# Optimization experiments

Hardware: AMD Instinct MI355X
Metric: run time of the kernel (lower is better)

Reference implementation:

```python
import jax, jax.numpy as jnp
import numpy as np

N_NODES = 20000
N_EDGES = 320000
F_IN = 256      # num_features_mol
HIDDEN = 512    # hidden_size


def _glorot(key, shape):
    fan_in, fan_out = shape
    lim = jnp.sqrt(6.0 / (fan_in + fan_out)).astype(jnp.float32)
    return jax.random.uniform(key, shape, jnp.float32, -lim, lim)


def setup_inputs() -> dict:
    key = jax.random.key(0)
    ks = jax.random.split(key, 12)
    x = jax.random.normal(ks[0], (N_NODES, F_IN), jnp.float32)
    edge_index = jax.random.randint(ks[1], (2, N_EDGES), 0, N_NODES, dtype=jnp.int64)
    d1, d2, d3 = F_IN * 2, F_IN * 2, F_IN * 4  # 512, 512, 1024
    return {
        "x": x,
        "edge_index": edge_index,
        # SAGEConv layer i: lin_l (neighbor, with bias), lin_r (root, no bias)
        "Wl1": _glorot(ks[2], (F_IN, d1)), "bl1": jnp.zeros((d1,), jnp.float32),
        "Wr1": _glorot(ks[3], (F_IN, d1)),
        "Wl2": _glorot(ks[4], (d1, d2)), "bl2": jnp.zeros((d2,), jnp.float32),
        "Wr2": _glorot(ks[5], (d1, d2)),
        "Wl3": _glorot(ks[6], (d2, d3)), "bl3": jnp.zeros((d3,), jnp.float32),
        "Wr3": _glorot(ks[7], (d2, d3)),
        # mol_fc_g1: Linear(4*F -> hidden)
        "Wfc": _glorot(ks[8], (d3, HIDDEN)), "bfc": jnp.zeros((HIDDEN,), jnp.float32),
    }


def _sage_mean(x, src, dst, Wl, bl, Wr):
    # mean-aggregate neighbor features: messages flow src -> dst
    msg = x[src]                                               # [E, d]
    agg = jax.ops.segment_sum(msg, dst, num_segments=N_NODES)  # [N, d]
    cnt = jax.ops.segment_sum(jnp.ones((src.shape[0],), x.dtype), dst,
                              num_segments=N_NODES)            # [N]
    mean = agg / jnp.maximum(cnt, 1.0)[:, None]                # zero-deg -> 0
    return mean @ Wl + bl + x @ Wr


def reference(x, edge_index, Wl1, bl1, Wr1, Wl2, bl2, Wr2, Wl3, bl3, Wr3, Wfc, bfc):
    src, dst = edge_index[0], edge_index[1]
    h = jax.nn.relu(_sage_mean(x, src, dst, Wl1, bl1, Wr1))
    h = jax.nn.relu(_sage_mean(h, src, dst, Wl2, bl2, Wr2))
    h = jax.nn.relu(_sage_mean(h, src, dst, Wl3, bl3, Wr3))
    return h @ Wfc + bfc                                       # [N, HIDDEN]
```

## Files before the change

### kernel.cpp

```cpp
#include <hip/hip_runtime.h>
#include <hip/hip_bf16.h>


typedef __bf16 bf16x8 __attribute__((ext_vector_type(8)));
typedef float  f32x4  __attribute__((ext_vector_type(4)));

#define N_NODES 20000
#define N_EDGES 320000

__device__ __forceinline__ int clampi(int v, int lo, int hi) {
    return v < lo ? lo : (v > hi ? hi : v);
}

__device__ __forceinline__ void load16_lds(const void* g, void* l) {
    __builtin_amdgcn_global_load_lds(
        (const __attribute__((address_space(1))) void*)g,
        (__attribute__((address_space(3))) void*)l, 16, 0, 0);
}


__global__ void k_count(const int* __restrict__ ei, int E, int* __restrict__ cnt) {
    int e = blockIdx.x * blockDim.x + threadIdx.x;
    if (e < E) {
        int dst = clampi(ei[E + e], 0, N_NODES - 1);
        atomicAdd(&cnt[dst], 1);
    }
}

__global__ __launch_bounds__(1024) void k_scan_block(const int* __restrict__ cnt,
                                                     int* __restrict__ off,
                                                     int* __restrict__ bsum, int n) {
    __shared__ int sm[1024];
    int b = blockIdx.x, tid = threadIdx.x;
    int i = b * 1024 + tid;
    int v = (i < n) ? cnt[i] : 0;
    sm[tid] = v;
    __syncthreads();
    for (int s = 1; s < 1024; s <<= 1) {
        int t = (tid >= s) ? sm[tid - s] : 0;
        __syncthreads();
        sm[tid] += t;
        __syncthreads();
    }
    if (i < n) off[i] = sm[tid] - v;
    if (tid == 1023) bsum[b] = sm[1023];
}

__global__ void k_scan_carry(const int* __restrict__ bsum, int* __restrict__ carry,
                             int nb, int* __restrict__ off, int n) {
    if (threadIdx.x == 0 && blockIdx.x == 0) {
        int acc = 0;
        for (int b = 0; b < nb; ++b) { carry[b] = acc; acc += bsum[b]; }
        off[n] = acc;
    }
}

__global__ __launch_bounds__(1024) void k_scan_add(int* __restrict__ off,
                                                   int* __restrict__ cur,
                                                   const int* __restrict__ carry, int n) {
    int i = blockIdx.x * 1024 + threadIdx.x;
    if (i < n) {
        int v = off[i] + carry[blockIdx.x];
        off[i] = v;
        cur[i] = v;
    }
}

__global__ void k_fill(const int* __restrict__ ei, int E,
                       int* __restrict__ cur, int* __restrict__ csr) {
    int e = blockIdx.x * blockDim.x + threadIdx.x;
    if (e < E) {
        int dst = clampi(ei[E + e], 0, N_NODES - 1);
        int src = clampi(ei[e], 0, N_NODES - 1);
        int pos = atomicAdd(&cur[dst], 1);
        if (pos >= 0 && pos < E) csr[pos] = src;
    }
}


__global__ void k_transpose_w(const float* __restrict__ W, int K, int N,
                              __hip_bfloat16* __restrict__ Wt, int ldt, int koff) {
    __shared__ float tile[32][33];
    int kb = blockIdx.y * 32, nb = blockIdx.x * 32;
    for (int i = 0; i < 32; i += 8) {
        int k = kb + threadIdx.y + i, n = nb + threadIdx.x;
        tile[threadIdx.y + i][threadIdx.x] = W[(size_t)k * N + n];
    }
    __syncthreads();
    for (int i = 0; i < 32; i += 8) {
        int n = nb + threadIdx.y + i, k = kb + threadIdx.x;
        Wt[(size_t)n * ldt + koff + k] = __float2bfloat16(tile[threadIdx.x][threadIdx.y + i]);
    }
}


__global__ __launch_bounds__(256) void k_agg_f32(const float* __restrict__ xin,
                                                 const int* __restrict__ off,
                                                 const int* __restrict__ csr,
                                                 __hip_bfloat16* __restrict__ outp,
                                                 int ostride) {
    __shared__ float sm[4][256];
    int node = blockIdx.x;
    int tid = threadIdx.x;
    int slot = tid >> 6, lane = tid & 63;
    int c0 = lane * 4;
    int beg = off[node], end = off[node + 1];
    float a0 = 0.f, a1 = 0.f, a2 = 0.f, a3 = 0.f;
    for (int e = beg + slot; e < end; e += 4) {
        int s = csr[e];
        float4 v = *(const float4*)(xin + (size_t)s * 256 + c0);
        a0 += v.x; a1 += v.y; a2 += v.z; a3 += v.w;
    }
    sm[slot][c0] = a0; sm[slot][c0 + 1] = a1; sm[slot][c0 + 2] = a2; sm[slot][c0 + 3] = a3;
    __syncthreads();
    float inv = 1.f / fmaxf((float)(end - beg), 1.f);
    float r = (sm[0][tid] + sm[1][tid]) + (sm[2][tid] + sm[3][tid]);
    outp[(size_t)node * ostride + tid] = __float2bfloat16(r * inv);
    outp[(size_t)node * ostride + 256 + tid] = __float2bfloat16(xin[(size_t)node * 256 + tid]);
}

__global__ __launch_bounds__(256) void k_agg_bf16(const __hip_bfloat16* __restrict__ hin,
                                                  int istride,
                                                  const int* __restrict__ off,
                                                  const int* __restrict__ csr,
                                                  __hip_bfloat16* __restrict__ outp,
                                                  int ostride) {
    __shared__ float sm[4][512];
    int node = blockIdx.x;
    int tid = threadIdx.x;
    int slot = tid >> 6, lane = tid & 63;
    int c0 = lane * 8;
    int beg = off[node], end = off[node + 1];
    float a[8] = {};
    for (int e = beg + slot; e < end; e += 4) {
        int s = csr[e];
        uint4 v = *(const uint4*)(hin + (size_t)s * istride + c0);
        const __hip_bfloat16* hb = (const __hip_bfloat16*)&v;
#pragma unroll
        for (int j = 0; j < 8; ++j) a[j] += __bfloat162float(hb[j]);
    }
#pragma unroll
    for (int j = 0; j < 8; ++j) sm[slot][c0 + j] = a[j];
    __syncthreads();
    float inv = 1.f / fmaxf((float)(end - beg), 1.f);
    int c = tid * 2;
    float r0 = (sm[0][c] + sm[1][c]) + (sm[2][c] + sm[3][c]);
    float r1 = (sm[0][c + 1] + sm[1][c + 1]) + (sm[2][c + 1] + sm[3][c + 1]);
    __hip_bfloat162 o;
    o.x = __float2bfloat16(r0 * inv);
    o.y = __float2bfloat16(r1 * inv);
    *(__hip_bfloat162*)(outp + (size_t)node * ostride + c) = o;
}


#define SMEM_BYTES 34816

template <bool RELU, bool OUT_BF16>
__global__ __launch_bounds__(256) void k_gemm_bt(const __hip_bfloat16* __restrict__ A,
                                                 int lda, int M, int K,
                                                 const __hip_bfloat16* __restrict__ Bt,
                                                 const float* __restrict__ bias,
                                                 __hip_bfloat16* __restrict__ obf,
                                                 float* __restrict__ of32,
                                                 int ldc, int coff,
                                                 int rtiles, int ctlog2) {
    __shared__ char smem[SMEM_BYTES];
    __bf16* Alds = (__bf16*)smem;
    __bf16* Blds = (__bf16*)(smem + 8192);

    int bid = blockIdx.x;
    int xcd = bid & 7, local = bid >> 3;
    int cmask = (1 << ctlog2) - 1;
    int colTile = local & cmask;
    int rowTile = (local >> ctlog2) * 8 + xcd;
    if (rowTile >= rtiles) return;
    int row0 = rowTile * 128, col0 = colTile * 128;

    int tid = threadIdx.x;
    int wave = tid >> 6, lane = tid & 63;
    int wr = wave >> 1, wc = wave & 1;
    int quad = lane >> 4, l16 = lane & 15;

    int rlo = lane >> 2, ch = lane & 3;
    int ra0 = clampi(row0 + wave * 32 + rlo, 0, M - 1);
    int ra1 = clampi(row0 + wave * 32 + 16 + rlo, 0, M - 1);
    const __hip_bfloat16* gA0 = A + (size_t)ra0 * lda + ch * 8;
    const __hip_bfloat16* gA1 = A + (size_t)ra1 * lda + ch * 8;
    const __hip_bfloat16* gB0 = Bt + (size_t)(col0 + wave * 32 + rlo) * K + ch * 8;
    const __hip_bfloat16* gB1 = gB0 + (size_t)16 * K;
    __bf16* lA0 = Alds + (wave * 32) * 32;
    __bf16* lA1 = Alds + (wave * 32 + 16) * 32;
    __bf16* lB0 = Blds + (wave * 32) * 32;
    __bf16* lB1 = Blds + (wave * 32 + 16) * 32;

    f32x4 acc[4][4] = {};

    for (int k0 = 0; k0 < K; k0 += 32) {
        __syncthreads();
        load16_lds(gA0 + k0, lA0);
        load16_lds(gA1 + k0, lA1);
        load16_lds(gB0 + k0, lB0);
        load16_lds(gB1 + k0, lB1);
        __syncthreads();

        bf16x8 af[4], bf[4];
#pragma unroll
        for (int mi = 0; mi < 4; ++mi)
            af[mi] = *(const bf16x8*)(Alds + (wr * 64 + mi * 16 + l16) * 32 + quad * 8);
#pragma unroll
        for (int ni = 0; ni < 4; ++ni)
            bf[ni] = *(const bf16x8*)(Blds + (wc * 64 + ni * 16 + l16) * 32 + quad * 8);
#pragma unroll
        for (int mi = 0; mi < 4; ++mi)
#pragma unroll
            for (int ni = 0; ni < 4; ++ni)
                acc[mi][ni] = __builtin_amdgcn_mfma_f32_16x16x32_bf16(af[mi], bf[ni],
                                                                      acc[mi][ni], 0, 0, 0);
    }

    __syncthreads();
    if (OUT_BF16) {
        __bf16* cb = (__bf16*)smem;
#pragma unroll
        for (int ni = 0; ni < 4; ++ni) {
            int ct = wc * 64 + ni * 16 + l16;
            float bv = bias[col0 + ct];
#pragma unroll
            for (int mi = 0; mi < 4; ++mi) {
                int rb = wr * 64 + mi * 16 + quad * 4;
#pragma unroll
                for (int r = 0; r < 4; ++r) {
                    float v = acc[mi][ni][r] + bv;
                    if (RELU) v = fmaxf(v, 0.f);
                    cb[(rb + r) * 136 + ct] = (__bf16)v;
                }
            }
        }
        __syncthreads();
        int chunk = tid & 15;
        int rl = tid >> 4;
#pragma unroll
        for (int p = 0; p < 8; ++p) {
            int rt = p * 16 + rl;
            int row = row0 + rt;
            if (row < M) {
                uint4 v = *(const uint4*)(cb + rt * 136 + chunk * 8);
                *(uint4*)(obf + (size_t)row * ldc + coff + col0 + chunk * 8) = v;
            }
        }
    } else {
        float* cf = (float*)smem;
#pragma unroll
        for (int h = 0; h < 2; ++h) {
            if (wc == h) {
#pragma unroll
                for (int ni = 0; ni < 4; ++ni) {
                    int ctl = ni * 16 + l16;
                    float bv = bias[col0 + h * 64 + ctl];
#pragma unroll
                    for (int mi = 0; mi < 4; ++mi) {
                        int rb = wr * 64 + mi * 16 + quad * 4;
#pragma unroll
                        for (int r = 0; r < 4; ++r) {
                            float v = acc[mi][ni][r] + bv;
                            if (RELU) v = fmaxf(v, 0.f);
                            cf[(rb + r) * 68 + ctl] = v;
                        }
                    }
                }
            }
            __syncthreads();
            int chunk = tid & 15;
            int rl = tid >> 4;
#pragma unroll
            for (int p = 0; p < 8; ++p) {
                int rt = p * 16 + rl;
                int row = row0 + rt;
                if (row < M) {
                    float4 v = *(const float4*)(cf + rt * 68 + chunk * 4);
                    *(float4*)(of32 + (size_t)row * ldc + col0 + h * 64 + chunk * 4) = v;
                }
            }
            __syncthreads();
        }
    }
}


extern "C" void kernel_launch(void* const* d_in, const int* in_sizes, int n_in,
                              void* d_out, int out_size, void* d_ws, size_t ws_size,
                              hipStream_t stream) {
    const float* x   = (const float*)d_in[0];
    const int*   ei  = (const int*)d_in[1];
    const float* Wl1 = (const float*)d_in[2];
    const float* bl1 = (const float*)d_in[3];
    const float* Wr1 = (const float*)d_in[4];
    const float* Wl2 = (const float*)d_in[5];
    const float* bl2 = (const float*)d_in[6];
    const float* Wr2 = (const float*)d_in[7];
    const float* Wl3 = (const float*)d_in[8];
    const float* bl3 = (const float*)d_in[9];
    const float* Wr3 = (const float*)d_in[10];
    const float* Wfc = (const float*)d_in[11];
    const float* bfc = (const float*)d_in[12];
    float* out = (float*)d_out;

    const int NN = N_NODES, E = N_EDGES;
    const int NB = (NN + 1023) / 1024;

    char* p = (char*)d_ws;
    auto alloc = [&](size_t bytes) {
        char* r = p;
        p += (bytes + 511) & ~(size_t)511;
        return r;
    };
    int* cnt   = (int*)alloc((size_t)NN * 4);
    int* off   = (int*)alloc((size_t)(NN + 1) * 4);
    int* cur   = (int*)alloc((size_t)NN * 4);
    int* csr   = (int*)alloc((size_t)E * 4);
    int* bsum  = (int*)alloc((size_t)NB * 4);
    int* carry = (int*)alloc((size_t)NB * 4);
    __hip_bfloat16* Acat1 = (__hip_bfloat16*)alloc((size_t)NN * 512 * 2);
    __hip_bfloat16* Acat2 = (__hip_bfloat16*)alloc((size_t)NN * 1024 * 2);
    __hip_bfloat16* Acat3 = (__hip_bfloat16*)alloc((size_t)NN * 1024 * 2);
    __hip_bfloat16* Wt1 = (__hip_bfloat16*)alloc((size_t)512 * 512 * 2);
    __hip_bfloat16* Wt2 = (__hip_bfloat16*)alloc((size_t)512 * 1024 * 2);
    __hip_bfloat16* Wt3 = (__hip_bfloat16*)alloc((size_t)1024 * 1024 * 2);
    __hip_bfloat16* Wt4 = (__hip_bfloat16*)alloc((size_t)512 * 1024 * 2);
    __hip_bfloat16* H3 = Acat2;

    hipMemsetAsync(cnt, 0, (size_t)NN * 4, stream);
    k_count<<<(E + 255) / 256, 256, 0, stream>>>(ei, E, cnt);
    k_scan_block<<<NB, 1024, 0, stream>>>(cnt, off, bsum, NN);
    k_scan_carry<<<1, 64, 0, stream>>>(bsum, carry, NB, off, NN);
    k_scan_add<<<NB, 1024, 0, stream>>>(off, cur, carry, NN);
    k_fill<<<(E + 255) / 256, 256, 0, stream>>>(ei, E, cur, csr);

    dim3 tb(32, 8);
    k_transpose_w<<<dim3(512 / 32, 256 / 32), tb, 0, stream>>>(Wl1, 256, 512, Wt1, 512, 0);
    k_transpose_w<<<dim3(512 / 32, 256 / 32), tb, 0, stream>>>(Wr1, 256, 512, Wt1, 512, 256);
    k_transpose_w<<<dim3(512 / 32, 512 / 32), tb, 0, stream>>>(Wl2, 512, 512, Wt2, 1024, 0);
    k_transpose_w<<<dim3(512 / 32, 512 / 32), tb, 0, stream>>>(Wr2, 512, 512, Wt2, 1024, 512);
    k_transpose_w<<<dim3(1024 / 32, 512 / 32), tb, 0, stream>>>(Wl3, 512, 1024, Wt3, 1024, 0);
    k_transpose_w<<<dim3(1024 / 32, 512 / 32), tb, 0, stream>>>(Wr3, 512, 1024, Wt3, 1024, 512);
    k_transpose_w<<<dim3(512 / 32, 1024 / 32), tb, 0, stream>>>(Wfc, 1024, 512, Wt4, 1024, 0);

    int rtiles = (NN + 127) / 128;
    int rg = ((rtiles + 7) / 8) * 8;

    k_agg_f32<<<NN, 256, 0, stream>>>(x, off, csr, Acat1, 512);
    k_gemm_bt<true, true><<<rg * 4, 256, 0, stream>>>(
        Acat1, 512, NN, 512, Wt1, bl1, Acat2, nullptr, 1024, 512, rtiles, 2);

    k_agg_bf16<<<NN, 256, 0, stream>>>(Acat2 + 512, 1024, off, csr, Acat2, 1024);
    k_gemm_bt<true, true><<<rg * 4, 256, 0, stream>>>(
        Acat2, 1024, NN, 1024, Wt2, bl2, Acat3, nullptr, 1024, 512, rtiles, 2);

    k_agg_bf16<<<NN, 256, 0, stream>>>(Acat3 + 512, 1024, off, csr, Acat3, 1024);
    k_gemm_bt<true, true><<<rg * 8, 256, 0, stream>>>(
        Acat3, 1024, NN, 1024, Wt3, bl3, H3, nullptr, 1024, 0, rtiles, 3);

    k_gemm_bt<false, false><<<rg * 4, 256, 0, stream>>>(
        H3, 1024, NN, 1024, Wt4, bfc, nullptr, out, 512, 0, rtiles, 2);
}
```

Baseline: 460.7 us.

## Store GEMM operands in pre-tiled k-chunked layout and merge weight transposes

```diff
diff --git a/kernel.cpp b/kernel.cpp
--- a/kernel.cpp
+++ b/kernel.cpp
@@ -7,6 +7,7 @@
 
 #define N_NODES 20000
 #define N_EDGES 320000
+#define MPAD 20096
 
 __device__ __forceinline__ int clampi(int v, int lo, int hi) {
     return v < lo ? lo : (v > hi ? hi : v);
@@ -21,10 +22,7 @@
 
 __global__ void k_count(const int* __restrict__ ei, int E, int* __restrict__ cnt) {
     int e = blockIdx.x * blockDim.x + threadIdx.x;
-    if (e < E) {
-        int dst = clampi(ei[E + e], 0, N_NODES - 1);
-        atomicAdd(&cnt[dst], 1);
-    }
+    if (e < E) atomicAdd(&cnt[clampi(ei[E + e], 0, N_NODES - 1)], 1);
 }
 
 __global__ __launch_bounds__(1024) void k_scan_block(const int* __restrict__ cnt,
@@ -78,18 +76,32 @@
 }
 
 
-__global__ void k_transpose_w(const float* __restrict__ W, int K, int N,
-                              __hip_bfloat16* __restrict__ Wt, int ldt, int koff) {
+struct TDesc { const float* W; __bf16* Wt; int K, N, KT, koff, tile0; };
+struct TDescs { TDesc d[7]; };
+
+__global__ void k_transpose_all(TDescs ds) {
     __shared__ float tile[32][33];
-    int kb = blockIdx.y * 32, nb = blockIdx.x * 32;
+    int b = blockIdx.x;
+    int di = 0;
+#pragma unroll
+    for (int i = 1; i < 7; ++i)
+        if (b >= ds.d[i].tile0) di = i;
+    const float* W = ds.d[di].W;
+    __bf16* Wt = ds.d[di].Wt;
+    int N = ds.d[di].N, KT = ds.d[di].KT, koff = ds.d[di].koff;
+    int t = b - ds.d[di].tile0;
+    int ntn = N >> 5;
+    int nb = (t % ntn) * 32, kb = (t / ntn) * 32;
     for (int i = 0; i < 32; i += 8) {
         int k = kb + threadIdx.y + i, n = nb + threadIdx.x;
         tile[threadIdx.y + i][threadIdx.x] = W[(size_t)k * N + n];
     }
     __syncthreads();
     for (int i = 0; i < 32; i += 8) {
-        int n = nb + threadIdx.y + i, k = kb + threadIdx.x;
-        Wt[(size_t)n * ldt + koff + k] = __float2bfloat16(tile[threadIdx.x][threadIdx.y + i]);
+        int n = nb + threadIdx.y + i, k = koff + kb + threadIdx.x;
+        size_t o = (size_t)(n >> 7) * ((size_t)KT * 128) + (size_t)(k >> 3) * 1024 +
+                   (size_t)((n & 127) * 8) + (k & 7);
+        Wt[o] = (__bf16)tile[threadIdx.x][threadIdx.y + i];
     }
 }
 
@@ -97,12 +109,10 @@
 __global__ __launch_bounds__(256) void k_agg_f32(const float* __restrict__ xin,
                                                  const int* __restrict__ off,
                                                  const int* __restrict__ csr,
-                                                 __hip_bfloat16* __restrict__ outp,
-                                                 int ostride) {
+                                                 __bf16* __restrict__ acat) {
     __shared__ float sm[4][256];
     int node = blockIdx.x;
-    int tid = threadIdx.x;
-    int slot = tid >> 6, lane = tid & 63;
+    int tid = threadIdx.x, slot = tid >> 6, lane = tid & 63;
     int c0 = lane * 4;
     int beg = off[node], end = off[node + 1];
     float a0 = 0.f, a1 = 0.f, a2 = 0.f, a3 = 0.f;
@@ -113,28 +123,40 @@
     }
     sm[slot][c0] = a0; sm[slot][c0 + 1] = a1; sm[slot][c0 + 2] = a2; sm[slot][c0 + 3] = a3;
     __syncthreads();
-    float inv = 1.f / fmaxf((float)(end - beg), 1.f);
-    float r = (sm[0][tid] + sm[1][tid]) + (sm[2][tid] + sm[3][tid]);
-    outp[(size_t)node * ostride + tid] = __float2bfloat16(r * inv);
-    outp[(size_t)node * ostride + 256 + tid] = __float2bfloat16(xin[(size_t)node * 256 + tid]);
-}
-
-__global__ __launch_bounds__(256) void k_agg_bf16(const __hip_bfloat16* __restrict__ hin,
-                                                  int istride,
+    __bf16* base = acat + (size_t)(node >> 7) * (512 * 128) + (size_t)((node & 127) * 8);
+    if (tid < 32) {
+        float inv = 1.f / fmaxf((float)(end - beg), 1.f);
+        int c = tid;
+        __bf16 tmp[8];
+#pragma unroll
+        for (int i = 0; i < 8; ++i) {
+            int col = c * 8 + i;
+            tmp[i] = (__bf16)((sm[0][col] + sm[1][col] + sm[2][col] + sm[3][col]) * inv);
+        }
+        *(uint4*)(base + (size_t)c * 1024) = *(const uint4*)tmp;
+    } else if (tid >= 64 && tid < 96) {
+        int c = tid - 64;
+        float4 u = *(const float4*)(xin + (size_t)node * 256 + c * 8);
+        float4 w = *(const float4*)(xin + (size_t)node * 256 + c * 8 + 4);
+        __bf16 tmp[8] = {(__bf16)u.x, (__bf16)u.y, (__bf16)u.z, (__bf16)u.w,
+                         (__bf16)w.x, (__bf16)w.y, (__bf16)w.z, (__bf16)w.w};
+        *(uint4*)(base + (size_t)(32 + c) * 1024) = *(const uint4*)tmp;
+    }
+}
+
+__global__ __launch_bounds__(256) void k_agg_bf16(const __hip_bfloat16* __restrict__ hrm,
                                                   const int* __restrict__ off,
                                                   const int* __restrict__ csr,
-                                                  __hip_bfloat16* __restrict__ outp,
-                                                  int ostride) {
+                                                  __bf16* __restrict__ acat) {
     __shared__ float sm[4][512];
     int node = blockIdx.x;
-    int tid = threadIdx.x;
-    int slot = tid >> 6, lane = tid & 63;
+    int tid = threadIdx.x, slot = tid >> 6, lane = tid & 63;
     int c0 = lane * 8;
     int beg = off[node], end = off[node + 1];
     float a[8] = {};
     for (int e = beg + slot; e < end; e += 4) {
         int s = csr[e];
-        uint4 v = *(const uint4*)(hin + (size_t)s * istride + c0);
+        uint4 v = *(const uint4*)(hrm + (size_t)s * 512 + c0);
         const __hip_bfloat16* hb = (const __hip_bfloat16*)&v;
 #pragma unroll
         for (int j = 0; j < 8; ++j) a[j] += __bfloat162float(hb[j]);
@@ -142,31 +164,33 @@
 #pragma unroll
     for (int j = 0; j < 8; ++j) sm[slot][c0 + j] = a[j];
     __syncthreads();
-    float inv = 1.f / fmaxf((float)(end - beg), 1.f);
-    int c = tid * 2;
-    float r0 = (sm[0][c] + sm[1][c]) + (sm[2][c] + sm[3][c]);
-    float r1 = (sm[0][c + 1] + sm[1][c + 1]) + (sm[2][c + 1] + sm[3][c + 1]);
-    __hip_bfloat162 o;
-    o.x = __float2bfloat16(r0 * inv);
-    o.y = __float2bfloat16(r1 * inv);
-    *(__hip_bfloat162*)(outp + (size_t)node * ostride + c) = o;
-}
-
-
-#define SMEM_BYTES 34816
-
-template <bool RELU, bool OUT_BF16>
-__global__ __launch_bounds__(256) void k_gemm_bt(const __hip_bfloat16* __restrict__ A,
-                                                 int lda, int M, int K,
-                                                 const __hip_bfloat16* __restrict__ Bt,
-                                                 const float* __restrict__ bias,
-                                                 __hip_bfloat16* __restrict__ obf,
-                                                 float* __restrict__ of32,
-                                                 int ldc, int coff,
-                                                 int rtiles, int ctlog2) {
-    __shared__ char smem[SMEM_BYTES];
+    if (tid < 64) {
+        float inv = 1.f / fmaxf((float)(end - beg), 1.f);
+        int c = tid;
+        __bf16 tmp[8];
+#pragma unroll
+        for (int i = 0; i < 8; ++i) {
+            int col = c * 8 + i;
+            tmp[i] = (__bf16)((sm[0][col] + sm[1][col] + sm[2][col] + sm[3][col]) * inv);
+        }
+        *(uint4*)(acat + (size_t)(node >> 7) * (1024 * 128) +
+                  (size_t)((node & 127) * 8) + (size_t)c * 1024) = *(const uint4*)tmp;
+    }
+}
+
+
+template <bool RELU, int OUTMODE>
+__global__ __launch_bounds__(256) void k_gemm(const __bf16* __restrict__ A, int K, int M,
+                                              const __bf16* __restrict__ B,
+                                              const float* __restrict__ bias,
+                                              __bf16* __restrict__ osw, int Kc, int coff,
+                                              __bf16* __restrict__ orm, int ldrm,
+                                              float* __restrict__ of32, int ldf,
+                                              int rtiles, int ctlog2) {
+    constexpr int SMEM = (OUTMODE == 2) ? 34816 : 32768;
+    __shared__ char smem[SMEM];
     __bf16* Alds = (__bf16*)smem;
-    __bf16* Blds = (__bf16*)(smem + 8192);
+    __bf16* Blds = (__bf16*)(smem + 16384);
 
     int bid = blockIdx.x;
     int xcd = bid & 7, local = bid >> 3;
@@ -174,52 +198,53 @@
     int colTile = local & cmask;
     int rowTile = (local >> ctlog2) * 8 + xcd;
     if (rowTile >= rtiles) return;
-    int row0 = rowTile * 128, col0 = colTile * 128;
+
+    const __bf16* Atile = A + (size_t)rowTile * ((size_t)K * 128);
+    const __bf16* Btile = B + (size_t)colTile * ((size_t)K * 128);
 
     int tid = threadIdx.x;
     int wave = tid >> 6, lane = tid & 63;
     int wr = wave >> 1, wc = wave & 1;
     int quad = lane >> 4, l16 = lane & 15;
 
-    int rlo = lane >> 2, ch = lane & 3;
-    int ra0 = clampi(row0 + wave * 32 + rlo, 0, M - 1);
-    int ra1 = clampi(row0 + wave * 32 + 16 + rlo, 0, M - 1);
-    const __hip_bfloat16* gA0 = A + (size_t)ra0 * lda + ch * 8;
-    const __hip_bfloat16* gA1 = A + (size_t)ra1 * lda + ch * 8;
-    const __hip_bfloat16* gB0 = Bt + (size_t)(col0 + wave * 32 + rlo) * K + ch * 8;
-    const __hip_bfloat16* gB1 = gB0 + (size_t)16 * K;
-    __bf16* lA0 = Alds + (wave * 32) * 32;
-    __bf16* lA1 = Alds + (wave * 32 + 16) * 32;
-    __bf16* lB0 = Blds + (wave * 32) * 32;
-    __bf16* lB1 = Blds + (wave * 32 + 16) * 32;
-
     f32x4 acc[4][4] = {};
 
-    for (int k0 = 0; k0 < K; k0 += 32) {
-        __syncthreads();
-        load16_lds(gA0 + k0, lA0);
-        load16_lds(gA1 + k0, lA1);
-        load16_lds(gB0 + k0, lB0);
-        load16_lds(gB1 + k0, lB1);
-        __syncthreads();
-
-        bf16x8 af[4], bf[4];
-#pragma unroll
-        for (int mi = 0; mi < 4; ++mi)
-            af[mi] = *(const bf16x8*)(Alds + (wr * 64 + mi * 16 + l16) * 32 + quad * 8);
-#pragma unroll
-        for (int ni = 0; ni < 4; ++ni)
-            bf[ni] = *(const bf16x8*)(Blds + (wc * 64 + ni * 16 + l16) * 32 + quad * 8);
-#pragma unroll
-        for (int mi = 0; mi < 4; ++mi)
+    for (int k0 = 0; k0 < K; k0 += 64) {
+        __syncthreads();
+        const __bf16* gA = Atile + (size_t)k0 * 128;
+        const __bf16* gB = Btile + (size_t)k0 * 128;
+#pragma unroll
+        for (int j = 0; j < 4; ++j) {
+            int slot = (j * 256 + tid) * 8;
+            load16_lds(gA + slot, Alds + slot);
+            load16_lds(gB + slot, Blds + slot);
+        }
+        __syncthreads();
+#pragma unroll
+        for (int sp = 0; sp < 2; ++sp) {
+            bf16x8 af[4], bf[4];
+#pragma unroll
+            for (int mi = 0; mi < 4; ++mi)
+                af[mi] = *(const bf16x8*)(Alds + sp * 4096 + quad * 1024 +
+                                          (wr * 64 + mi * 16 + l16) * 8);
 #pragma unroll
             for (int ni = 0; ni < 4; ++ni)
-                acc[mi][ni] = __builtin_amdgcn_mfma_f32_16x16x32_bf16(af[mi], bf[ni],
-                                                                      acc[mi][ni], 0, 0, 0);
-    }
-
-    __syncthreads();
-    if (OUT_BF16) {
+                bf[ni] = *(const bf16x8*)(Blds + sp * 4096 + quad * 1024 +
+                                          (wc * 64 + ni * 16 + l16) * 8);
+#pragma unroll
+            for (int mi = 0; mi < 4; ++mi)
+#pragma unroll
+                for (int ni = 0; ni < 4; ++ni)
+                    acc[mi][ni] = __builtin_amdgcn_mfma_f32_16x16x32_bf16(
+                        af[mi], bf[ni], acc[mi][ni], 0, 0, 0);
+        }
+    }
+
+    int col0 = colTile * 128;
+    int row0 = rowTile * 128;
+    __syncthreads();
+
+    if (OUTMODE != 2) {
         __bf16* cb = (__bf16*)smem;
 #pragma unroll
         for (int ni = 0; ni < 4; ++ni) {
@@ -232,20 +257,25 @@
                 for (int r = 0; r < 4; ++r) {
                     float v = acc[mi][ni][r] + bv;
                     if (RELU) v = fmaxf(v, 0.f);
-                    cb[(rb + r) * 136 + ct] = (__bf16)v;
+                    cb[(ct >> 3) * 1024 + (rb + r) * 8 + (ct & 7)] = (__bf16)v;
                 }
             }
         }
         __syncthreads();
-        int chunk = tid & 15;
-        int rl = tid >> 4;
-#pragma unroll
-        for (int p = 0; p < 8; ++p) {
-            int rt = p * 16 + rl;
-            int row = row0 + rt;
-            if (row < M) {
-                uint4 v = *(const uint4*)(cb + rt * 136 + chunk * 8);
-                *(uint4*)(obf + (size_t)row * ldc + coff + col0 + chunk * 8) = v;
+        __bf16* dst = osw + (size_t)rowTile * ((size_t)Kc * 128) +
+                      (size_t)((coff + col0) >> 3) * 1024;
+#pragma unroll
+        for (int p2 = 0; p2 < 8; ++p2) {
+            int idx = (p2 * 256 + tid) * 8;
+            *(uint4*)(dst + idx) = *(const uint4*)(cb + idx);
+        }
+        if (OUTMODE == 1) {
+#pragma unroll
+            for (int p2 = 0; p2 < 8; ++p2) {
+                int rr = p2 * 16 + (tid >> 4);
+                int cc = tid & 15;
+                *(uint4*)(orm + (size_t)(row0 + rr) * ldrm + col0 + cc * 8) =
+                    *(const uint4*)(cb + cc * 1024 + rr * 8);
             }
         }
     } else {
@@ -270,15 +300,14 @@
                 }
             }
             __syncthreads();
-            int chunk = tid & 15;
-            int rl = tid >> 4;
-#pragma unroll
-            for (int p = 0; p < 8; ++p) {
-                int rt = p * 16 + rl;
+            int chunk = tid & 15, rl = tid >> 4;
+#pragma unroll
+            for (int p2 = 0; p2 < 8; ++p2) {
+                int rt = p2 * 16 + rl;
                 int row = row0 + rt;
                 if (row < M) {
                     float4 v = *(const float4*)(cf + rt * 68 + chunk * 4);
-                    *(float4*)(of32 + (size_t)row * ldc + col0 + h * 64 + chunk * 4) = v;
+                    *(float4*)(of32 + (size_t)row * ldf + col0 + h * 64 + chunk * 4) = v;
                 }
             }
             __syncthreads();
@@ -320,14 +349,15 @@
     int* csr   = (int*)alloc((size_t)E * 4);
     int* bsum  = (int*)alloc((size_t)NB * 4);
     int* carry = (int*)alloc((size_t)NB * 4);
-    __hip_bfloat16* Acat1 = (__hip_bfloat16*)alloc((size_t)NN * 512 * 2);
-    __hip_bfloat16* Acat2 = (__hip_bfloat16*)alloc((size_t)NN * 1024 * 2);
-    __hip_bfloat16* Acat3 = (__hip_bfloat16*)alloc((size_t)NN * 1024 * 2);
-    __hip_bfloat16* Wt1 = (__hip_bfloat16*)alloc((size_t)512 * 512 * 2);
-    __hip_bfloat16* Wt2 = (__hip_bfloat16*)alloc((size_t)512 * 1024 * 2);
-    __hip_bfloat16* Wt3 = (__hip_bfloat16*)alloc((size_t)1024 * 1024 * 2);
-    __hip_bfloat16* Wt4 = (__hip_bfloat16*)alloc((size_t)512 * 1024 * 2);
-    __hip_bfloat16* H3 = Acat2;
+    __bf16* Acat1 = (__bf16*)alloc((size_t)MPAD * 512 * 2);
+    __bf16* Acat2 = (__bf16*)alloc((size_t)MPAD * 1024 * 2);
+    __bf16* Acat3 = (__bf16*)alloc((size_t)MPAD * 1024 * 2);
+    __bf16* Hrm   = (__bf16*)alloc((size_t)MPAD * 512 * 2);
+    __bf16* Wt1 = (__bf16*)alloc((size_t)512 * 512 * 2);
+    __bf16* Wt2 = (__bf16*)alloc((size_t)512 * 1024 * 2);
+    __bf16* Wt3 = (__bf16*)alloc((size_t)1024 * 1024 * 2);
+    __bf16* Wt4 = (__bf16*)alloc((size_t)512 * 1024 * 2);
+    __bf16* H3 = Acat2;
 
     hipMemsetAsync(cnt, 0, (size_t)NN * 4, stream);
     k_count<<<(E + 255) / 256, 256, 0, stream>>>(ei, E, cnt);
@@ -336,30 +366,31 @@
     k_scan_add<<<NB, 1024, 0, stream>>>(off, cur, carry, NN);
     k_fill<<<(E + 255) / 256, 256, 0, stream>>>(ei, E, cur, csr);
 
-    dim3 tb(32, 8);
-    k_transpose_w<<<dim3(512 / 32, 256 / 32), tb, 0, stream>>>(Wl1, 256, 512, Wt1, 512, 0);
-    k_transpose_w<<<dim3(512 / 32, 256 / 32), tb, 0, stream>>>(Wr1, 256, 512, Wt1, 512, 256);
-    k_transpose_w<<<dim3(512 / 32, 512 / 32), tb, 0, stream>>>(Wl2, 512, 512, Wt2, 1024, 0);
-    k_transpose_w<<<dim3(512 / 32, 512 / 32), tb, 0, stream>>>(Wr2, 512, 512, Wt2, 1024, 512);
-    k_transpose_w<<<dim3(1024 / 32, 512 / 32), tb, 0, stream>>>(Wl3, 512, 1024, Wt3, 1024, 0);
-    k_transpose_w<<<dim3(1024 / 32, 512 / 32), tb, 0, stream>>>(Wr3, 512, 1024, Wt3, 1024, 512);
-    k_transpose_w<<<dim3(512 / 32, 1024 / 32), tb, 0, stream>>>(Wfc, 1024, 512, Wt4, 1024, 0);
+    TDescs td;
+    td.d[0] = {Wl1, Wt1, 256, 512, 512, 0, 0};
+    td.d[1] = {Wr1, Wt1, 256, 512, 512, 256, 128};
+    td.d[2] = {Wl2, Wt2, 512, 512, 1024, 0, 256};
+    td.d[3] = {Wr2, Wt2, 512, 512, 1024, 512, 512};
+    td.d[4] = {Wl3, Wt3, 512, 1024, 1024, 0, 768};
+    td.d[5] = {Wr3, Wt3, 512, 1024, 1024, 512, 1280};
+    td.d[6] = {Wfc, Wt4, 1024, 512, 1024, 0, 1792};
+    k_transpose_all<<<2304, dim3(32, 8), 0, stream>>>(td);
 
     int rtiles = (NN + 127) / 128;
     int rg = ((rtiles + 7) / 8) * 8;
 
-    k_agg_f32<<<NN, 256, 0, stream>>>(x, off, csr, Acat1, 512);
-    k_gemm_bt<true, true><<<rg * 4, 256, 0, stream>>>(
-        Acat1, 512, NN, 512, Wt1, bl1, Acat2, nullptr, 1024, 512, rtiles, 2);
-
-    k_agg_bf16<<<NN, 256, 0, stream>>>(Acat2 + 512, 1024, off, csr, Acat2, 1024);
-    k_gemm_bt<true, true><<<rg * 4, 256, 0, stream>>>(
-        Acat2, 1024, NN, 1024, Wt2, bl2, Acat3, nullptr, 1024, 512, rtiles, 2);
-
-    k_agg_bf16<<<NN, 256, 0, stream>>>(Acat3 + 512, 1024, off, csr, Acat3, 1024);
-    k_gemm_bt<true, true><<<rg * 8, 256, 0, stream>>>(
-        Acat3, 1024, NN, 1024, Wt3, bl3, H3, nullptr, 1024, 0, rtiles, 3);
-
-    k_gemm_bt<false, false><<<rg * 4, 256, 0, stream>>>(
-        H3, 1024, NN, 1024, Wt4, bfc, nullptr, out, 512, 0, rtiles, 2);
-}
+    k_agg_f32<<<NN, 256, 0, stream>>>(x, off, csr, Acat1);
+    k_gemm<true, 1><<<rg * 4, 256, 0, stream>>>(
+        Acat1, 512, NN, Wt1, bl1, Acat2, 1024, 512, Hrm, 512, nullptr, 0, rtiles, 2);
+
+    k_agg_bf16<<<NN, 256, 0, stream>>>((const __hip_bfloat16*)Hrm, off, csr, Acat2);
+    k_gemm<true, 1><<<rg * 4, 256, 0, stream>>>(
+        Acat2, 1024, NN, Wt2, bl2, Acat3, 1024, 512, Hrm, 512, nullptr, 0, rtiles, 2);
+
+    k_agg_bf16<<<NN, 256, 0, stream>>>((const __hip_bfloat16*)Hrm, off, csr, Acat3);
+    k_gemm<true, 0><<<rg * 8, 256, 0, stream>>>(
+        Acat3, 1024, NN, Wt3, bl3, H3, 1024, 0, nullptr, 0, nullptr, 0, rtiles, 3);
+
+    k_gemm<false, 2><<<rg * 4, 256, 0, stream>>>(
+        H3, 1024, NN, Wt4, bfc, nullptr, 0, 0, nullptr, 0, out, 512, rtiles, 2);
+}
```

After: 446.4 us. 3.1% less time.
